# Performance work log

Hardware: AMD Instinct MI355X
Metric: run time of the kernel (lower is better)

## Reference

```python
import jax, jax.numpy as jnp
import numpy as np

B, NQ, NK, E, H, F, L = 8, 300, 4096, 256, 8, 2048, 6
D = E // H
SCALE = D ** -0.5


def _ln(x, g, b):
    m = x.mean(-1, keepdims=True)
    v = ((x - m) ** 2).mean(-1, keepdims=True)
    return (x - m) / jnp.sqrt(v + 1e-5) * g + b


def _split_heads(x):
    b, n, _ = x.shape
    return x.reshape(b, n, H, D).transpose(0, 2, 1, 3)  # (B,H,N,D)


def _merge_heads(x):
    b, h, n, d = x.shape
    return x.transpose(0, 2, 1, 3).reshape(b, n, h * d)


def setup_inputs() -> dict:
    key = jax.random.key(0)
    c = [0]
    def nk():
        c[0] += 1
        return jax.random.fold_in(key, c[0])
    def p(shape):
        return jax.random.normal(nk(), shape, jnp.float32) * 0.02
    return {
        "tgt": jax.random.normal(nk(), (B, NQ, E), jnp.float32),
        "memory": jax.random.normal(nk(), (B, NK, E), jnp.float32),
        "geometry_mask": jax.random.randint(nk(), (B, NQ, NK), 0, 2).astype(bool),
        "sa_wqkv": p((L, 3 * E, E)), "sa_bqkv": p((L, 3 * E)),
        "sa_wo": p((L, E, E)), "sa_bo": p((L, E)),
        "ca_wq": p((L, E, E)), "ca_bq": p((L, E)),
        "ca_wk": p((L, E, E)), "ca_bk": p((L, E)),
        "ca_wv": p((L, E, E)), "ca_bv": p((L, E)),
        "ca_wo": p((L, E, E)), "ca_bo": p((L, E)),
        "f_w1": p((L, F, E)), "f_b1": p((L, F)),
        "f_w2": p((L, E, F)), "f_b2": p((L, E)),
        "ln1g": jnp.ones((L, E)), "ln1b": jnp.zeros((L, E)),
        "ln2g": jnp.ones((L, E)), "ln2b": jnp.zeros((L, E)),
        "ln3g": jnp.ones((L, E)), "ln3b": jnp.zeros((L, E)),
        "lnfg": jnp.ones((E,)), "lnfb": jnp.zeros((E,)),
    }


def _forward(tgt, memory, geometry_mask, params):
    mask4 = geometry_mask[:, None, :, :]  # (B,1,NQ,NK), broadcast over heads

    def step(t, p):
        (wqkv, bqkv, wo, bo, wq, bq, wk, bk, wv, bv, wco, bco,
         w1, b1, w2, b2, g1, be1, g2, be2, g3, be3) = p
        # --- self-attention (torch nn.MultiheadAttention, eval mode) ---
        qkv = t @ wqkv.T + bqkv
        q, k, v = jnp.split(qkv, 3, axis=-1)
        q, k, v = _split_heads(q), _split_heads(k), _split_heads(v)
        a = jax.nn.softmax(jnp.einsum('bhqd,bhkd->bhqk', q, k) * SCALE, axis=-1)
        sa = _merge_heads(jnp.einsum('bhqk,bhkd->bhqd', a, v)) @ wo.T + bo
        t = _ln(t + sa, g1, be1)
        # --- geometry-constrained cross-attention ---
        q = _split_heads(t @ wq.T + bq)
        k = _split_heads(memory @ wk.T + bk)
        v = _split_heads(memory @ wv.T + bv)
        s = jnp.einsum('bhqd,bhkd->bhqk', q, k) * SCALE
        s = jnp.where(mask4, s, -jnp.inf)  # masked_fill(~mask, -inf)
        a = jax.nn.softmax(s, axis=-1)
        ca = _merge_heads(jnp.einsum('bhqk,bhkd->bhqd', a, v)) @ wco.T + bco
        t = _ln(t + ca, g2, be2)
        # --- FFN ---
        f = jax.nn.relu(t @ w1.T + b1) @ w2.T + b2
        t = _ln(t + f, g3, be3)
        return t, None

    out, _ = jax.lax.scan(step, tgt, params)
    return out


def reference(tgt, memory, geometry_mask, sa_wqkv, sa_bqkv, sa_wo, sa_bo,
              ca_wq, ca_bq, ca_wk, ca_bk, ca_wv, ca_bv, ca_wo, ca_bo,
              f_w1, f_b1, f_w2, f_b2, ln1g, ln1b, ln2g, ln2b, ln3g, ln3b,
              lnfg, lnfb):
    params = (sa_wqkv, sa_bqkv, sa_wo, sa_bo, ca_wq, ca_bq, ca_wk, ca_bk,
              ca_wv, ca_bv, ca_wo, ca_bo, f_w1, f_b1, f_w2, f_b2,
              ln1g, ln1b, ln2g, ln2b, ln3g, ln3b)
    out = _forward(tgt, memory, geometry_mask, params)
    return _ln(out, lnfg, lnfb)
```

## Files before the change

kernel.cpp:

```cpp
#include <hip/hip_runtime.h>
#include <hip/hip_bf16.h>

constexpr int cB = 8, cNQ = 300, cNK = 4096, cE = 256, cH = 8, cD = 32, cF = 2048, cL = 6;
constexpr int MT = cB * cNQ;
constexpr int MM = cB * cNK;
constexpr int cQT = 10;
constexpr int cKS = 4;
constexpr float kScale = 0.17677669529663687f;

typedef __attribute__((ext_vector_type(8))) short short8_t;
typedef __attribute__((ext_vector_type(4))) short short4_t;
typedef __attribute__((ext_vector_type(4))) float float4_t;

__device__ inline short f2bf(float x) {
  __hip_bfloat16 h = __float2bfloat16(x);
  return __builtin_bit_cast(short, h);
}

__global__ void init_t(const float* __restrict__ in, float* __restrict__ t,
                       __hip_bfloat16* __restrict__ tb, int n) {
  int i = blockIdx.x * 256 + threadIdx.x;
  if (i < n) { float v = in[i]; t[i] = v; tb[i] = __float2bfloat16(v); }
}
__global__ void cast_f32_bf16(const float* __restrict__ in, __hip_bfloat16* __restrict__ out, int n) {
  int i = blockIdx.x * 256 + threadIdx.x;
  if (i < n) out[i] = __float2bfloat16(in[i]);
}

__global__ void pack_mask_T(const int* __restrict__ m, unsigned* __restrict__ mT) {
  int key = blockIdx.x * 256 + threadIdx.x;
  int qt = blockIdx.y, b = blockIdx.z;
  unsigned w = 0;
  for (int j = 0; j < 32; ++j) {
    int q = qt * 32 + j;
    unsigned bit = (q < cNQ) ? (unsigned)(m[((size_t)b * cNQ + q) * cNK + key] != 0) : 0u;
    w |= bit << j;
  }
  mT[((size_t)b * cQT + qt) * cNK + key] = w;
}

template<typename TA, typename TW, int EPI, int OMODE, typename TOUT>
__global__ __launch_bounds__(256) void gemm_mfma(const TA* __restrict__ A,
                                                 const TW* __restrict__ W,
                                                 const float* __restrict__ bias,
                                                 TOUT* __restrict__ C,
                                                 int M, int N, int K) {
  constexpr int LDSS = 72;
  __shared__ short As[64][LDSS];
  __shared__ short Ws[64][LDSS];
  int tid = threadIdx.x;
  int bm = blockIdx.x * 64, bn = blockIdx.y * 64;
  int lane = tid & 63, wave = tid >> 6;
  int m16 = lane & 15, quad = lane >> 4;
  int wm = (wave >> 1) * 32, wn = (wave & 1) * 32;

  int srow = tid >> 2;
  int kc = (tid & 3) * 16;
  bool aok = (bm + srow) < M;

  float4_t acc[2][2];
#pragma unroll
  for (int i = 0; i < 2; ++i)
#pragma unroll
    for (int j = 0; j < 2; ++j) acc[i][j] = (float4_t){0.f, 0.f, 0.f, 0.f};

  for (int k0 = 0; k0 < K; k0 += 64) {
    if constexpr (__hip_internal::is_same<TA, float>::value) {
      const float* src = A + (size_t)(bm + srow) * K + k0 + kc;
      short8_t p0, p1;
#pragma unroll
      for (int u = 0; u < 8; ++u) p0[u] = aok ? f2bf(src[u]) : (short)0;
#pragma unroll
      for (int u = 0; u < 8; ++u) p1[u] = aok ? f2bf(src[8 + u]) : (short)0;
      *(short8_t*)&As[srow][kc] = p0;
      *(short8_t*)&As[srow][kc + 8] = p1;
    } else {
      const TA* src = A + (size_t)(bm + srow) * K + k0 + kc;
      short8_t z = 0;
      *(short8_t*)&As[srow][kc] = aok ? *(const short8_t*)src : z;
      *(short8_t*)&As[srow][kc + 8] = aok ? *(const short8_t*)(src + 8) : z;
    }
    if constexpr (__hip_internal::is_same<TW, float>::value) {
      const float* src = W + (size_t)(bn + srow) * K + k0 + kc;
      short8_t p0, p1;
#pragma unroll
      for (int u = 0; u < 8; ++u) p0[u] = f2bf(src[u]);
#pragma unroll
      for (int u = 0; u < 8; ++u) p1[u] = f2bf(src[8 + u]);
      *(short8_t*)&Ws[srow][kc] = p0;
      *(short8_t*)&Ws[srow][kc + 8] = p1;
    } else {
      const TW* src = W + (size_t)(bn + srow) * K + k0 + kc;
      *(short8_t*)&Ws[srow][kc] = *(const short8_t*)src;
      *(short8_t*)&Ws[srow][kc + 8] = *(const short8_t*)(src + 8);
    }
    __syncthreads();
#pragma unroll
    for (int kk = 0; kk < 2; ++kk) {
      short8_t aF[2], bF[2];
#pragma unroll
      for (int i = 0; i < 2; ++i)
        aF[i] = *(const short8_t*)&As[wm + i * 16 + m16][kk * 32 + quad * 8];
#pragma unroll
      for (int j = 0; j < 2; ++j)
        bF[j] = *(const short8_t*)&Ws[wn + j * 16 + m16][kk * 32 + quad * 8];
#pragma unroll
      for (int i = 0; i < 2; ++i)
#pragma unroll
        for (int j = 0; j < 2; ++j)
          acc[i][j] = __builtin_amdgcn_mfma_f32_16x16x32_bf16(aF[i], bF[j], acc[i][j], 0, 0, 0);
    }
    __syncthreads();
  }

  if constexpr (OMODE == 2) {
#pragma unroll
    for (int i = 0; i < 2; ++i)
#pragma unroll
      for (int r = 0; r < 4; ++r) {
        int ml = wm + i * 16 + quad * 4 + r;
#pragma unroll
        for (int j = 0; j < 2; ++j) {
          int nl = wn + j * 16 + m16;
          Ws[nl][ml] = f2bf(acc[i][j][r] + bias[bn + nl]);
        }
      }
    __syncthreads();
    int nl = tid >> 2, mc = (tid & 3) * 16;
    if (bm + mc < M) {
      int n = bn + nl;
      __hip_bfloat16* dst = (__hip_bfloat16*)C +
          ((size_t)(n >> 5) * 32 + (n & 31)) * (size_t)M + bm + mc;
      *(short8_t*)dst = *(const short8_t*)&Ws[nl][mc];
      *(short8_t*)(dst + 8) = *(const short8_t*)&Ws[nl][mc + 8];
    }
  } else {
#pragma unroll
    for (int i = 0; i < 2; ++i) {
#pragma unroll
      for (int r = 0; r < 4; ++r) {
        int m = bm + wm + i * 16 + quad * 4 + r;
        if (m >= M) continue;
#pragma unroll
        for (int j = 0; j < 2; ++j) {
          int n = bn + wn + j * 16 + m16;
          float v = acc[i][j][r] + bias[n];
          if (EPI == 1) v = fmaxf(v, 0.f);
          if constexpr (OMODE == 1) {
            ((__hip_bfloat16*)C)[((size_t)(n >> 5) * M + m) * 32 + (n & 31)] = __float2bfloat16(v);
          } else if constexpr (__hip_internal::is_same<TOUT, float>::value) {
            C[(size_t)m * N + n] = v;
          } else {
            C[(size_t)m * N + n] = __float2bfloat16(v);
          }
        }
      }
    }
  }
}

template<typename TW, int EPI, int OMODE, typename TOUT>
__global__ __launch_bounds__(256) void gemm128(const __hip_bfloat16* __restrict__ A,
                                               const TW* __restrict__ W,
                                               const float* __restrict__ bias,
                                               TOUT* __restrict__ C,
                                               int M, int N, int K) {
  __shared__ short lds[2 * 128 * 72];
  auto As = (short(*)[72])lds;
  auto Ws = (short(*)[72])(lds + 128 * 72);
  int tid = threadIdx.x;
  int bm = blockIdx.x * 128, bn = blockIdx.y * 128;
  int lane = tid & 63, wave = tid >> 6;
  int n16 = lane & 15, quad = lane >> 4;
  int wm = (wave >> 1) * 64, wn = (wave & 1) * 64;
  int srow = tid >> 1, kc = (tid & 1) * 32;
  bool aok = (bm + srow) < M;

  float4_t acc[4][4];
#pragma unroll
  for (int i = 0; i < 4; ++i)
#pragma unroll
    for (int j = 0; j < 4; ++j) acc[i][j] = (float4_t){0.f, 0.f, 0.f, 0.f};

  for (int k0 = 0; k0 < K; k0 += 64) {
    {
      const __hip_bfloat16* src = A + (size_t)(bm + srow) * K + k0 + kc;
      short8_t z = 0;
#pragma unroll
      for (int u = 0; u < 4; ++u)
        *(short8_t*)&As[srow][kc + u * 8] = aok ? *(const short8_t*)(src + u * 8) : z;
    }
    if constexpr (__hip_internal::is_same<TW, float>::value) {
      const float* src = W + (size_t)(bn + srow) * K + k0 + kc;
#pragma unroll
      for (int u = 0; u < 4; ++u) {
        short8_t p;
#pragma unroll
        for (int v = 0; v < 8; ++v) p[v] = f2bf(src[u * 8 + v]);
        *(short8_t*)&Ws[srow][kc + u * 8] = p;
      }
    } else {
      const TW* src = W + (size_t)(bn + srow) * K + k0 + kc;
#pragma unroll
      for (int u = 0; u < 4; ++u)
        *(short8_t*)&Ws[srow][kc + u * 8] = *(const short8_t*)(src + u * 8);
    }
    __syncthreads();
#pragma unroll
    for (int kk = 0; kk < 2; ++kk) {
      short8_t aF[4], bF[4];
#pragma unroll
      for (int i = 0; i < 4; ++i)
        aF[i] = *(const short8_t*)&As[wm + i * 16 + n16][kk * 32 + quad * 8];
#pragma unroll
      for (int j = 0; j < 4; ++j)
        bF[j] = *(const short8_t*)&Ws[wn + j * 16 + n16][kk * 32 + quad * 8];
#pragma unroll
      for (int i = 0; i < 4; ++i)
#pragma unroll
        for (int j = 0; j < 4; ++j)
          acc[i][j] = __builtin_amdgcn_mfma_f32_16x16x32_bf16(aF[i], bF[j], acc[i][j], 0, 0, 0);
    }
    __syncthreads();
  }

  if constexpr (OMODE == 2) {
    auto TT = (short(*)[128])lds;
#pragma unroll
    for (int i = 0; i < 4; ++i)
#pragma unroll
      for (int r = 0; r < 4; ++r) {
        int ml = wm + i * 16 + quad * 4 + r;
#pragma unroll
        for (int j = 0; j < 4; ++j) {
          int nl = wn + j * 16 + n16;
          TT[nl][ml] = f2bf(acc[i][j][r] + bias[bn + nl]);
        }
      }
    __syncthreads();
    int nl = tid >> 1, mh = (tid & 1) * 64;
    int n = bn + nl;
    __hip_bfloat16* dst = (__hip_bfloat16*)C +
        ((size_t)(n >> 5) * 32 + (n & 31)) * (size_t)M + bm + mh;
#pragma unroll
    for (int ch = 0; ch < 8; ++ch) {
      if (bm + mh + ch * 8 < M)
        *(short8_t*)(dst + ch * 8) = *(const short8_t*)&TT[nl][mh + ch * 8];
    }
  } else {
#pragma unroll
    for (int i = 0; i < 4; ++i) {
#pragma unroll
      for (int r = 0; r < 4; ++r) {
        int m = bm + wm + i * 16 + quad * 4 + r;
        if (m >= M) continue;
#pragma unroll
        for (int j = 0; j < 4; ++j) {
          int n = bn + wn + j * 16 + n16;
          float v = acc[i][j][r] + bias[n];
          if (EPI == 1) v = fmaxf(v, 0.f);
          if constexpr (OMODE == 1) {
            ((__hip_bfloat16*)C)[((size_t)(n >> 5) * M + m) * 32 + (n & 31)] = __float2bfloat16(v);
          } else if constexpr (__hip_internal::is_same<TOUT, float>::value) {
            C[(size_t)m * N + n] = v;
          } else {
            C[(size_t)m * N + n] = __float2bfloat16(v);
          }
        }
      }
    }
  }
}

template<typename TQ, bool MASKED>
__global__ __launch_bounds__(64, 4) void attn_flash(
    const TQ* __restrict__ qb, size_t strQb, size_t strQh, int qRowStr,
    const __hip_bfloat16* __restrict__ kb, size_t strKb, size_t strKh, int kRowStr,
    const __hip_bfloat16* __restrict__ vt, size_t strVb, size_t strVh, size_t strVd,
    const unsigned* __restrict__ mT, size_t strMb,
    float* __restrict__ pO, size_t pStrO,
    float* __restrict__ pL, size_t pStrL,
    int nq, int nk, int kChunk) {
  int hb = blockIdx.x;
  int h = hb & 7, bz = hb >> 3;
  int qt = blockIdx.y, ks = blockIdx.z;
  int qbase = qt * 32;

  const TQ* q = qb + (size_t)bz * strQb + (size_t)h * strQh;
  const __hip_bfloat16* K = kb + (size_t)bz * strKb + (size_t)h * strKh;
  const __hip_bfloat16* V = vt + (size_t)bz * strVb + (size_t)h * strVh;
  const unsigned* mrow = MASKED ? (mT + (size_t)bz * strMb + (size_t)qt * cNK) : nullptr;

  int lane = threadIdx.x;
  int n16 = lane & 15, quad = lane >> 4;

  __shared__ short sP[32][40];

  short8_t qf[2];
#pragma unroll
  for (int qi = 0; qi < 2; ++qi) {
    qf[qi] = 0;
    int qr = qbase + qi * 16 + n16;
    if (qr < nq) {
      const TQ* qp = q + (size_t)qr * qRowStr + quad * 8;
      if constexpr (__hip_internal::is_same<TQ, float>::value) {
#pragma unroll
        for (int j = 0; j < 8; ++j) qf[qi][j] = f2bf(qp[j]);
      } else {
        qf[qi] = *(const short8_t*)qp;
      }
    }
  }
  short8_t ones;
#pragma unroll
  for (int j = 0; j < 8; ++j) ones[j] = f2bf(1.0f);

  float4_t accO[2][2], accL[2];
#pragma unroll
  for (int qi = 0; qi < 2; ++qi) {
    accL[qi] = (float4_t){0.f, 0.f, 0.f, 0.f};
#pragma unroll
    for (int di = 0; di < 2; ++di) accO[qi][di] = (float4_t){0.f, 0.f, 0.f, 0.f};
  }
  float4_t zero4 = {0.f, 0.f, 0.f, 0.f};

  int kbeg = ks * kChunk;
  int kend = kbeg + kChunk;
  if (kend > ((nk + 31) & ~31)) kend = (nk + 31) & ~31;
  for (int koff = kbeg; koff < kend; koff += 32) {
    int k0 = koff + 2 * n16;
    unsigned w0 = 0xFFFFFFFFu, w1 = 0xFFFFFFFFu;
    if (MASKED) {
      const unsigned* mp = mrow + k0;
      w0 = mp[0]; w1 = mp[1];
    }
    bool in0 = k0 < nk, in1 = (k0 + 1) < nk;
    short8_t kf0 = *(const short8_t*)(K + (size_t)k0 * kRowStr + quad * 8);
    short8_t kf1 = *(const short8_t*)(K + (size_t)(k0 + 1) * kRowStr + quad * 8);
    short8_t vf0 = *(const short8_t*)(V + (size_t)n16 * strVd + koff + quad * 8);
    short8_t vf1 = *(const short8_t*)(V + (size_t)(16 + n16) * strVd + koff + quad * 8);
    float4_t s00 = __builtin_amdgcn_mfma_f32_16x16x32_bf16(qf[0], kf0, zero4, 0, 0, 0);
    float4_t s01 = __builtin_amdgcn_mfma_f32_16x16x32_bf16(qf[0], kf1, zero4, 0, 0, 0);
    float4_t s10 = __builtin_amdgcn_mfma_f32_16x16x32_bf16(qf[1], kf0, zero4, 0, 0, 0);
    float4_t s11 = __builtin_amdgcn_mfma_f32_16x16x32_bf16(qf[1], kf1, zero4, 0, 0, 0);
#pragma unroll
    for (int qi = 0; qi < 2; ++qi) {
      const float4_t& sa = qi ? s10 : s00;
      const float4_t& sb = qi ? s11 : s01;
#pragma unroll
      for (int r = 0; r < 4; ++r) {
        int row = qi * 16 + quad * 4 + r;
        bool ok0 = in0, ok1 = in1;
        if (MASKED) {
          ok0 = ok0 && ((w0 >> row) & 1u);
          ok1 = ok1 && ((w1 >> row) & 1u);
        }
        float p0 = ok0 ? __expf(sa[r] * kScale) : 0.f;
        float p1 = ok1 ? __expf(sb[r] * kScale) : 0.f;
        unsigned pw = (unsigned)(unsigned short)f2bf(p0) |
                      ((unsigned)(unsigned short)f2bf(p1) << 16);
        *(unsigned*)&sP[row][2 * n16] = pw;
      }
    }
#pragma unroll
    for (int qi = 0; qi < 2; ++qi) {
      short8_t pf = *(const short8_t*)&sP[qi * 16 + n16][quad * 8];
      accO[qi][0] = __builtin_amdgcn_mfma_f32_16x16x32_bf16(pf, vf0, accO[qi][0], 0, 0, 0);
      accO[qi][1] = __builtin_amdgcn_mfma_f32_16x16x32_bf16(pf, vf1, accO[qi][1], 0, 0, 0);
      accL[qi]    = __builtin_amdgcn_mfma_f32_16x16x32_bf16(pf, ones, accL[qi], 0, 0, 0);
    }
  }

  size_t oBase = (size_t)ks * pStrO + (size_t)(bz * cNQ) * 256 + h * 32;
  size_t lBase = (size_t)ks * pStrL + (size_t)hb * 320;
#pragma unroll
  for (int qi = 0; qi < 2; ++qi) {
#pragma unroll
    for (int r = 0; r < 4; ++r) {
      int row = qi * 16 + quad * 4 + r;
      if (qbase + row >= nq) continue;
#pragma unroll
      for (int di = 0; di < 2; ++di)
        pO[oBase + (size_t)(qbase + row) * 256 + di * 16 + n16] = accO[qi][di][r];
      if (n16 == 0) pL[lBase + qbase + row] = accL[qi][r];
    }
  }
}

__global__ __launch_bounds__(64) void attn_merge(const float* __restrict__ pO,
                                                 const float* __restrict__ pL,
                                                 __hip_bfloat16* __restrict__ out) {
  int row = blockIdx.x;
  int lane = threadIdx.x;
  int c0 = lane * 4;
  int bz = row / cNQ, qq = row - bz * cNQ;
  int h = c0 >> 5;
  float l = 0.f;
#pragma unroll
  for (int ks = 0; ks < cKS; ++ks)
    l += pL[(size_t)ks * (64 * 320) + (size_t)(bz * 8 + h) * 320 + qq];
  float inv = 1.f / l;
  float o[4] = {0.f, 0.f, 0.f, 0.f};
#pragma unroll
  for (int ks = 0; ks < cKS; ++ks) {
    const float4_t v = *(const float4_t*)&pO[(size_t)ks * (MT * 256) + (size_t)row * 256 + c0];
#pragma unroll
    for (int u = 0; u < 4; ++u) o[u] += v[u];
  }
  short4_t res = {f2bf(o[0] * inv), f2bf(o[1] * inv), f2bf(o[2] * inv), f2bf(o[3] * inv)};
  *(short4_t*)&out[(size_t)row * 256 + c0] = res;
}

__global__ __launch_bounds__(64) void add_ln_k(float* __restrict__ t,
                                               __hip_bfloat16* __restrict__ tb,
                                               const float* __restrict__ delta,
                                               const float* __restrict__ g,
                                               const float* __restrict__ bb) {
  int r = blockIdx.x, lane = threadIdx.x;
  size_t base = (size_t)r * cE + lane * 4;
  float x[4];
  float s = 0.f;
#pragma unroll
  for (int i = 0; i < 4; ++i) { x[i] = t[base + i] + delta[base + i]; s += x[i]; }
  for (int off = 32; off; off >>= 1) s += __shfl_xor(s, off);
  float mean = s * (1.f / cE);
  float v = 0.f;
#pragma unroll
  for (int i = 0; i < 4; ++i) { float dd = x[i] - mean; v += dd * dd; }
  for (int off = 32; off; off >>= 1) v += __shfl_xor(v, off);
  float rstd = rsqrtf(v * (1.f / cE) + 1e-5f);
  float y[4];
#pragma unroll
  for (int i = 0; i < 4; ++i) {
    y[i] = (x[i] - mean) * rstd * g[lane * 4 + i] + bb[lane * 4 + i];
    t[base + i] = y[i];
  }
  short4_t pb = {f2bf(y[0]), f2bf(y[1]), f2bf(y[2]), f2bf(y[3])};
  *(short4_t*)&tb[base] = pb;
}

__global__ __launch_bounds__(64) void final_ln_k(const float* __restrict__ t,
                                                 const float* __restrict__ g,
                                                 const float* __restrict__ bb,
                                                 float* __restrict__ out) {
  int r = blockIdx.x, lane = threadIdx.x;
  size_t base = (size_t)r * cE + lane * 4;
  float x[4];
  float s = 0.f;
#pragma unroll
  for (int i = 0; i < 4; ++i) { x[i] = t[base + i]; s += x[i]; }
  for (int off = 32; off; off >>= 1) s += __shfl_xor(s, off);
  float mean = s * (1.f / cE);
  float v = 0.f;
#pragma unroll
  for (int i = 0; i < 4; ++i) { float dd = x[i] - mean; v += dd * dd; }
  for (int off = 32; off; off >>= 1) v += __shfl_xor(v, off);
  float rstd = rsqrtf(v * (1.f / cE) + 1e-5f);
#pragma unroll
  for (int i = 0; i < 4; ++i)
    out[base + i] = (x[i] - mean) * rstd * g[lane * 4 + i] + bb[lane * 4 + i];
}

struct Bufs {
  float *t, *s1, *s2, *pO, *pL;
  __hip_bfloat16 *tb, *big2, *vtq, *s1b, *s2b, *qbf, *ffnh, *kbuf, *vtb, *membf;
  unsigned* mTr;
  const float* memory;
  bool fullKV, precast;
};

template<typename TW>
static void run_layers(const TW* const* wt, const float* const* bs,
                       const float* ln1g, const float* ln1b,
                       const float* ln2g, const float* ln2b,
                       const float* ln3g, const float* ln3b,
                       Bufs B, hipStream_t stream) {
  const size_t pStrO = (size_t)MT * 256, pStrL = 64 * 320;
  for (int l = 0; l < cL; ++l) {
    const TW* wqkv = wt[0] + (size_t)l * 3 * cE * cE;  const float* bqkv = bs[0] + (size_t)l * 3 * cE;
    const TW* wo   = wt[1] + (size_t)l * cE * cE;      const float* bo   = bs[1] + (size_t)l * cE;
    const TW* wq   = wt[2] + (size_t)l * cE * cE;      const float* bq   = bs[2] + (size_t)l * cE;
    const TW* wk   = wt[3] + (size_t)l * cE * cE;      const float* bk   = bs[3] + (size_t)l * cE;
    const TW* wv   = wt[4] + (size_t)l * cE * cE;      const float* bv   = bs[4] + (size_t)l * cE;
    const TW* wco  = wt[5] + (size_t)l * cE * cE;      const float* bco  = bs[5] + (size_t)l * cE;
    const TW* w1   = wt[6] + (size_t)l * cF * cE;      const float* b1   = bs[6] + (size_t)l * cF;
    const TW* w2   = wt[7] + (size_t)l * cE * cF;      const float* b2   = bs[7] + (size_t)l * cE;

    gemm_mfma<__hip_bfloat16, TW, 0, 0, __hip_bfloat16><<<dim3(38, 8), 256, 0, stream>>>(
        B.tb, wqkv, bqkv, B.big2, MT, 512, cE);
    gemm_mfma<__hip_bfloat16, TW, 0, 2, __hip_bfloat16><<<dim3(38, 4), 256, 0, stream>>>(
        B.tb, wqkv + (size_t)512 * cE, bqkv + 512, B.vtq, MT, cE, cE);
    attn_flash<__hip_bfloat16, false><<<dim3(64, cQT, cKS), 64, 0, stream>>>(
        B.big2, (size_t)cNQ * 512, 32, 512,
        B.big2 + 256, (size_t)cNQ * 512, 32, 512,
        B.vtq, 300, (size_t)cD * MT, MT,
        nullptr, 0,
        B.pO, pStrO, B.pL, pStrL, cNQ, cNQ, 96);
    attn_merge<<<MT, 64, 0, stream>>>(B.pO, B.pL, B.s1b);
    gemm_mfma<__hip_bfloat16, TW, 0, 0, float><<<dim3(38, 4), 256, 0, stream>>>(
        B.s1b, wo, bo, B.s2, MT, cE, cE);
    add_ln_k<<<MT, 64, 0, stream>>>(B.t, B.tb, B.s2, ln1g + (size_t)l * cE, ln1b + (size_t)l * cE);
    gemm_mfma<__hip_bfloat16, TW, 0, 0, __hip_bfloat16><<<dim3(38, 4), 256, 0, stream>>>(
        B.tb, wq, bq, B.qbf, MT, cE, cE);
    if (B.fullKV && B.precast) {
      gemm128<TW, 0, 1, __hip_bfloat16><<<dim3(256, 2), 256, 0, stream>>>(
          B.membf, wk, bk, B.kbuf, MM, cE, cE);
      gemm128<TW, 0, 2, __hip_bfloat16><<<dim3(256, 2), 256, 0, stream>>>(
          B.membf, wv, bv, B.vtb, MM, cE, cE);
      attn_flash<__hip_bfloat16, true><<<dim3(64, cQT, cKS), 64, 0, stream>>>(
          B.qbf, (size_t)cNQ * cE, 32, cE,
          B.kbuf, (size_t)cNK * cD, (size_t)MM * cD, cD,
          B.vtb, (size_t)cNK, (size_t)cD * MM, MM,
          B.mTr, (size_t)cQT * cNK,
          B.pO, pStrO, B.pL, pStrL, cNQ, cNK, 1024);
      attn_merge<<<MT, 64, 0, stream>>>(B.pO, B.pL, B.s2b);
    } else {
      for (int b = 0; b < cB; ++b) {
        const float* memb = B.memory + (size_t)b * cNK * cE;
        gemm_mfma<float, TW, 0, 1, __hip_bfloat16><<<dim3(64, 4), 256, 0, stream>>>(
            memb, wk, bk, B.kbuf, cNK, cE, cE);
        gemm_mfma<float, TW, 0, 2, __hip_bfloat16><<<dim3(64, 4), 256, 0, stream>>>(
            memb, wv, bv, B.vtb, cNK, cE, cE);
        attn_flash<__hip_bfloat16, true><<<dim3(8, cQT, cKS), 64, 0, stream>>>(
            B.qbf + (size_t)b * cNQ * cE, 0, 32, cE,
            B.kbuf, 0, (size_t)cNK * cD, cD,
            B.vtb, 0, (size_t)cD * cNK, cNK,
            B.mTr + (size_t)b * cQT * cNK, 0,
            B.pO + (size_t)b * cNQ * 256, pStrO, B.pL + (size_t)b * 8 * 320, pStrL,
            cNQ, cNK, 1024);
      }
      attn_merge<<<MT, 64, 0, stream>>>(B.pO, B.pL, B.s2b);
    }
    gemm_mfma<__hip_bfloat16, TW, 0, 0, float><<<dim3(38, 4), 256, 0, stream>>>(
        B.s2b, wco, bco, B.s1, MT, cE, cE);
    add_ln_k<<<MT, 64, 0, stream>>>(B.t, B.tb, B.s1, ln2g + (size_t)l * cE, ln2b + (size_t)l * cE);
    gemm128<TW, 1, 0, __hip_bfloat16><<<dim3(19, 16), 256, 0, stream>>>(
        B.tb, w1, b1, B.ffnh, MT, cF, cE);
    gemm_mfma<__hip_bfloat16, TW, 0, 0, float><<<dim3(38, 4), 256, 0, stream>>>(
        B.ffnh, w2, b2, B.s1, MT, cE, cF);
    add_ln_k<<<MT, 64, 0, stream>>>(B.t, B.tb, B.s1, ln3g + (size_t)l * cE, ln3b + (size_t)l * cE);
  }
}

extern "C" void kernel_launch(void* const* d_in, const int* in_sizes, int n_in,
                              void* d_out, int out_size, void* d_ws, size_t ws_size,
                              hipStream_t stream) {
  (void)in_sizes; (void)n_in; (void)out_size;
  const float* tgt    = (const float*)d_in[0];
  const float* memory = (const float*)d_in[1];
  const int*   gmask  = (const int*)d_in[2];
  const float* w_in[8]  = {(const float*)d_in[3], (const float*)d_in[5], (const float*)d_in[7],
                           (const float*)d_in[9], (const float*)d_in[11], (const float*)d_in[13],
                           (const float*)d_in[15], (const float*)d_in[17]};
  const float* b_in[8]  = {(const float*)d_in[4], (const float*)d_in[6], (const float*)d_in[8],
                           (const float*)d_in[10], (const float*)d_in[12], (const float*)d_in[14],
                           (const float*)d_in[16], (const float*)d_in[18]};
  const size_t w_sz[8]  = {(size_t)cL*3*cE*cE, (size_t)cL*cE*cE, (size_t)cL*cE*cE,
                           (size_t)cL*cE*cE, (size_t)cL*cE*cE, (size_t)cL*cE*cE,
                           (size_t)cL*cF*cE, (size_t)cL*cE*cF};
  const float* ln1g = (const float*)d_in[19], *ln1b = (const float*)d_in[20];
  const float* ln2g = (const float*)d_in[21], *ln2b = (const float*)d_in[22];
  const float* ln3g = (const float*)d_in[23], *ln3b = (const float*)d_in[24];
  const float* lnfg = (const float*)d_in[25], *lnfb = (const float*)d_in[26];

  char* wp = (char*)d_ws;
  auto alloc = [&](size_t bytes) { void* p = wp; wp += (bytes + 255) & ~(size_t)255; return p; };

  Bufs B;
  B.memory = memory;
  B.t  = (float*)alloc((size_t)MT * cE * 4);
  B.s1 = (float*)alloc((size_t)MT * cE * 4);
  B.s2 = (float*)alloc((size_t)MT * cE * 4);
  B.tb = (__hip_bfloat16*)alloc((size_t)MT * cE * 2);
  B.big2 = (__hip_bfloat16*)alloc((size_t)MT * 512 * 2);
  B.vtq  = (__hip_bfloat16*)alloc((size_t)cH * cD * MT * 2);
  B.mTr = (unsigned*)alloc((size_t)cB * cQT * cNK * 4);
  B.pO = (float*)alloc((size_t)cKS * MT * 256 * 4);
  B.pL = (float*)alloc((size_t)cKS * 64 * 320 * 4);
  B.s1b = B.big2;
  B.s2b = B.big2 + (size_t)MT * 256;
  B.qbf = (__hip_bfloat16*)B.s1;
  B.ffnh = (__hip_bfloat16*)B.pO;

  size_t kvFull = (size_t)cH * MM * cD * 2;
  size_t used = (size_t)(wp - (char*)d_ws);
  B.fullKV = ws_size >= used + 2 * kvFull;
  if (B.fullKV) {
    B.kbuf = (__hip_bfloat16*)alloc(kvFull);
    B.vtb  = (__hip_bfloat16*)alloc(kvFull);
  } else {
    B.kbuf = (__hip_bfloat16*)alloc((size_t)cH * cNK * cD * 2);
    B.vtb  = (__hip_bfloat16*)alloc((size_t)cH * cNK * cD * 2);
  }
  size_t memBytes = (size_t)MM * cE * 2;
  used = (size_t)(wp - (char*)d_ws);
  B.precast = B.fullKV && (ws_size >= used + memBytes);
  B.membf = B.precast ? (__hip_bfloat16*)alloc(memBytes) : nullptr;

  size_t wbfTotal = 0;
  for (int i = 0; i < 8; ++i) wbfTotal += ((w_sz[i] * 2 + 255) & ~(size_t)255);
  used = (size_t)(wp - (char*)d_ws);
  bool wPre = ws_size >= used + wbfTotal;
  __hip_bfloat16* wbf[8] = {};
  if (wPre)
    for (int i = 0; i < 8; ++i) wbf[i] = (__hip_bfloat16*)alloc(w_sz[i] * 2);

  init_t<<<(MT * cE + 255) / 256, 256, 0, stream>>>(tgt, B.t, B.tb, MT * cE);
  pack_mask_T<<<dim3(cNK / 256, cQT, cB), 256, 0, stream>>>(gmask, B.mTr);
  if (B.precast)
    cast_f32_bf16<<<(MM * cE + 255) / 256, 256, 0, stream>>>(memory, B.membf, MM * cE);
  if (wPre)
    for (int i = 0; i < 8; ++i)
      cast_f32_bf16<<<(int)((w_sz[i] + 255) / 256), 256, 0, stream>>>(w_in[i], wbf[i], (int)w_sz[i]);

  if (wPre) {
    const __hip_bfloat16* wt[8];
    for (int i = 0; i < 8; ++i) wt[i] = wbf[i];
    run_layers<__hip_bfloat16>(wt, b_in, ln1g, ln1b, ln2g, ln2b, ln3g, ln3b, B, stream);
  } else {
    run_layers<float>(w_in, b_in, ln1g, ln1b, ln2g, ln2b, ln3g, ln3b, B, stream);
  }

  final_ln_k<<<MT, 64, 0, stream>>>(B.t, lnfg, lnfb, (float*)d_out);
}
```

Measured before the change: 1.268 ms.

## Fuse split-K attention merge into output GEMM, merge K/V GEMMs, prefetch attention tiles

Removes the separate attn_merge kernel by having the output-projection GEMM sum partial O and L across key splits and normalize while loading its A tile. It also merges the K and V projection GEMMs into one launch, raises the cross-attention key-split count from 4 to 8 with smaller chunks, and software-prefetches the next K/V/mask fragments in the flash loop. The exponent becomes exp2 with a folded constant, and bf16 packing uses integer rounding. These aim to cut launch count, intermediate traffic and load latency, at the cost of larger partial buffers and redundant merge work repeated across the N-blocks of the GEMM.

New measurement: 1.409 ms. 11.1% more time.

```diff
diff --git a/kernel.cpp b/kernel.cpp
--- a/kernel.cpp
+++ b/kernel.cpp
@@ -5,8 +5,12 @@
 constexpr int MT = cB * cNQ;
 constexpr int MM = cB * cNK;
 constexpr int cQT = 10;
-constexpr int cKS = 4;
+constexpr int cKSc = 8;
+constexpr int cKSs = 4;
 constexpr float kScale = 0.17677669529663687f;
+constexpr float kE = 0.25509966355953075f;
+constexpr size_t pStrO = (size_t)MT * 256;
+constexpr size_t pStrL = 64 * 320;
 
 typedef __attribute__((ext_vector_type(8))) short short8_t;
 typedef __attribute__((ext_vector_type(4))) short short4_t;
@@ -39,12 +43,13 @@
   mT[((size_t)b * cQT + qt) * cNK + key] = w;
 }
 
-template<typename TA, typename TW, int EPI, int OMODE, typename TOUT>
+template<typename TA, typename TW, int EPI, int OMODE, typename TOUT, int NKS>
 __global__ __launch_bounds__(256) void gemm_mfma(const TA* __restrict__ A,
                                                  const TW* __restrict__ W,
                                                  const float* __restrict__ bias,
                                                  TOUT* __restrict__ C,
-                                                 int M, int N, int K) {
+                                                 int M, int N, int K,
+                                                 const float* __restrict__ pL) {
   constexpr int LDSS = 72;
   __shared__ short As[64][LDSS];
   __shared__ short Ws[64][LDSS];
@@ -65,7 +70,37 @@
     for (int j = 0; j < 2; ++j) acc[i][j] = (float4_t){0.f, 0.f, 0.f, 0.f};
 
   for (int k0 = 0; k0 < K; k0 += 64) {
-    if constexpr (__hip_internal::is_same<TA, float>::value) {
+    if constexpr (NKS > 0) {
+      const float* pO = (const float*)A;
+      short8_t p0 = 0, p1 = 0;
+      if (aok) {
+        int m = bm + srow;
+        int bz = m / cNQ, qq = m - bz * cNQ;
+        int h = (k0 + kc) >> 5;
+        float l = 0.f;
+#pragma unroll
+        for (int ks = 0; ks < NKS; ++ks)
+          l += pL[(size_t)ks * pStrL + (size_t)(bz * 8 + h) * 320 + qq];
+        float inv = 1.f / l;
+        float v[16];
+#pragma unroll
+        for (int c = 0; c < 4; ++c) {
+          float4_t sum = {0.f, 0.f, 0.f, 0.f};
+#pragma unroll
+          for (int ks = 0; ks < NKS; ++ks) {
+            float4_t x = *(const float4_t*)&pO[(size_t)ks * pStrO + (size_t)m * 256 + k0 + kc + c * 4];
+#pragma unroll
+            for (int u = 0; u < 4; ++u) sum[u] += x[u];
+          }
+#pragma unroll
+          for (int u = 0; u < 4; ++u) v[c * 4 + u] = sum[u] * inv;
+        }
+#pragma unroll
+        for (int u = 0; u < 8; ++u) { p0[u] = f2bf(v[u]); p1[u] = f2bf(v[8 + u]); }
+      }
+      *(short8_t*)&As[srow][kc] = p0;
+      *(short8_t*)&As[srow][kc + 8] = p1;
+    } else if constexpr (__hip_internal::is_same<TA, float>::value) {
       const float* src = A + (size_t)(bm + srow) * K + k0 + kc;
       short8_t p0, p1;
 #pragma unroll
@@ -159,7 +194,7 @@
   }
 }
 
-template<typename TW, int EPI, int OMODE, typename TOUT>
+template<typename TW, int EPI, typename TOUT>
 __global__ __launch_bounds__(256) void gemm128(const __hip_bfloat16* __restrict__ A,
                                                const TW* __restrict__ W,
                                                const float* __restrict__ bias,
@@ -224,7 +259,105 @@
     __syncthreads();
   }
 
-  if constexpr (OMODE == 2) {
+#pragma unroll
+  for (int i = 0; i < 4; ++i) {
+#pragma unroll
+    for (int r = 0; r < 4; ++r) {
+      int m = bm + wm + i * 16 + quad * 4 + r;
+      if (m >= M) continue;
+#pragma unroll
+      for (int j = 0; j < 4; ++j) {
+        int n = bn + wn + j * 16 + n16;
+        float v = acc[i][j][r] + bias[n];
+        if (EPI == 1) v = fmaxf(v, 0.f);
+        if constexpr (__hip_internal::is_same<TOUT, float>::value)
+          C[(size_t)m * N + n] = v;
+        else
+          C[(size_t)m * N + n] = __float2bfloat16(v);
+      }
+    }
+  }
+}
+
+template<typename TA, typename TW>
+__global__ __launch_bounds__(256) void gemm_kv(const TA* __restrict__ A,
+                                               const TW* __restrict__ Wk, const TW* __restrict__ Wv,
+                                               const float* __restrict__ bk, const float* __restrict__ bv,
+                                               __hip_bfloat16* __restrict__ Ck,
+                                               __hip_bfloat16* __restrict__ Cv,
+                                               int M, int K) {
+  __shared__ short lds[2 * 128 * 72];
+  auto As = (short(*)[72])lds;
+  auto Ws = (short(*)[72])(lds + 128 * 72);
+  bool isV = blockIdx.z == 1;
+  const TW* W = isV ? Wv : Wk;
+  const float* bias = isV ? bv : bk;
+  int tid = threadIdx.x;
+  int bm = blockIdx.x * 128, bn = blockIdx.y * 128;
+  int lane = tid & 63, wave = tid >> 6;
+  int n16 = lane & 15, quad = lane >> 4;
+  int wm = (wave >> 1) * 64, wn = (wave & 1) * 64;
+  int srow = tid >> 1, kc = (tid & 1) * 32;
+  bool aok = (bm + srow) < M;
+
+  float4_t acc[4][4];
+#pragma unroll
+  for (int i = 0; i < 4; ++i)
+#pragma unroll
+    for (int j = 0; j < 4; ++j) acc[i][j] = (float4_t){0.f, 0.f, 0.f, 0.f};
+
+  for (int k0 = 0; k0 < K; k0 += 64) {
+    if constexpr (__hip_internal::is_same<TA, float>::value) {
+      const float* src = A + (size_t)(bm + srow) * K + k0 + kc;
+#pragma unroll
+      for (int u = 0; u < 4; ++u) {
+        short8_t p;
+#pragma unroll
+        for (int v = 0; v < 8; ++v) p[v] = aok ? f2bf(src[u * 8 + v]) : (short)0;
+        *(short8_t*)&As[srow][kc + u * 8] = p;
+      }
+    } else {
+      const TA* src = A + (size_t)(bm + srow) * K + k0 + kc;
+      short8_t z = 0;
+#pragma unroll
+      for (int u = 0; u < 4; ++u)
+        *(short8_t*)&As[srow][kc + u * 8] = aok ? *(const short8_t*)(src + u * 8) : z;
+    }
+    if constexpr (__hip_internal::is_same<TW, float>::value) {
+      const float* src = W + (size_t)(bn + srow) * K + k0 + kc;
+#pragma unroll
+      for (int u = 0; u < 4; ++u) {
+        short8_t p;
+#pragma unroll
+        for (int v = 0; v < 8; ++v) p[v] = f2bf(src[u * 8 + v]);
+        *(short8_t*)&Ws[srow][kc + u * 8] = p;
+      }
+    } else {
+      const TW* src = W + (size_t)(bn + srow) * K + k0 + kc;
+#pragma unroll
+      for (int u = 0; u < 4; ++u)
+        *(short8_t*)&Ws[srow][kc + u * 8] = *(const short8_t*)(src + u * 8);
+    }
+    __syncthreads();
+#pragma unroll
+    for (int kk = 0; kk < 2; ++kk) {
+      short8_t aF[4], bF[4];
+#pragma unroll
+      for (int i = 0; i < 4; ++i)
+        aF[i] = *(const short8_t*)&As[wm + i * 16 + n16][kk * 32 + quad * 8];
+#pragma unroll
+      for (int j = 0; j < 4; ++j)
+        bF[j] = *(const short8_t*)&Ws[wn + j * 16 + n16][kk * 32 + quad * 8];
+#pragma unroll
+      for (int i = 0; i < 4; ++i)
+#pragma unroll
+        for (int j = 0; j < 4; ++j)
+          acc[i][j] = __builtin_amdgcn_mfma_f32_16x16x32_bf16(aF[i], bF[j], acc[i][j], 0, 0, 0);
+    }
+    __syncthreads();
+  }
+
+  if (isV) {
     auto TT = (short(*)[128])lds;
 #pragma unroll
     for (int i = 0; i < 4; ++i)
@@ -240,8 +373,7 @@
     __syncthreads();
     int nl = tid >> 1, mh = (tid & 1) * 64;
     int n = bn + nl;
-    __hip_bfloat16* dst = (__hip_bfloat16*)C +
-        ((size_t)(n >> 5) * 32 + (n & 31)) * (size_t)M + bm + mh;
+    __hip_bfloat16* dst = Cv + ((size_t)(n >> 5) * 32 + (n & 31)) * (size_t)M + bm + mh;
 #pragma unroll
     for (int ch = 0; ch < 8; ++ch) {
       if (bm + mh + ch * 8 < M)
@@ -258,14 +390,7 @@
         for (int j = 0; j < 4; ++j) {
           int n = bn + wn + j * 16 + n16;
           float v = acc[i][j][r] + bias[n];
-          if (EPI == 1) v = fmaxf(v, 0.f);
-          if constexpr (OMODE == 1) {
-            ((__hip_bfloat16*)C)[((size_t)(n >> 5) * M + m) * 32 + (n & 31)] = __float2bfloat16(v);
-          } else if constexpr (__hip_internal::is_same<TOUT, float>::value) {
-            C[(size_t)m * N + n] = v;
-          } else {
-            C[(size_t)m * N + n] = __float2bfloat16(v);
-          }
+          Ck[((size_t)(n >> 5) * M + m) * 32 + (n & 31)] = __float2bfloat16(v);
         }
       }
     }
@@ -278,8 +403,7 @@
     const __hip_bfloat16* __restrict__ kb, size_t strKb, size_t strKh, int kRowStr,
     const __hip_bfloat16* __restrict__ vt, size_t strVb, size_t strVh, size_t strVd,
     const unsigned* __restrict__ mT, size_t strMb,
-    float* __restrict__ pO, size_t pStrO,
-    float* __restrict__ pL, size_t pStrL,
+    float* __restrict__ pO, float* __restrict__ pL,
     int nq, int nk, int kChunk) {
   int hb = blockIdx.x;
   int h = hb & 7, bz = hb >> 3;
@@ -324,25 +448,43 @@
   }
   float4_t zero4 = {0.f, 0.f, 0.f, 0.f};
 
+  const __hip_bfloat16* Vb0 = V + (size_t)n16 * strVd;
+  const __hip_bfloat16* Vb1 = V + (size_t)(16 + n16) * strVd;
+
   int kbeg = ks * kChunk;
   int kend = kbeg + kChunk;
-  if (kend > ((nk + 31) & ~31)) kend = (nk + 31) & ~31;
+  int nkAl = (nk + 31) & ~31;
+  if (kend > nkAl) kend = nkAl;
+
+  short8_t kfA = 0, kfB = 0, vfA = 0, vfB = 0;
+  unsigned mwA = ~0u, mwB = ~0u;
+  if (kbeg < kend) {
+    int k0i = kbeg + 2 * n16;
+    kfA = *(const short8_t*)(K + (size_t)k0i * kRowStr + quad * 8);
+    kfB = *(const short8_t*)(K + (size_t)(k0i + 1) * kRowStr + quad * 8);
+    vfA = *(const short8_t*)(Vb0 + kbeg + quad * 8);
+    vfB = *(const short8_t*)(Vb1 + kbeg + quad * 8);
+    if (MASKED) { mwA = mrow[k0i]; mwB = mrow[k0i + 1]; }
+  }
+
   for (int koff = kbeg; koff < kend; koff += 32) {
-    int k0 = koff + 2 * n16;
-    unsigned w0 = 0xFFFFFFFFu, w1 = 0xFFFFFFFFu;
-    if (MASKED) {
-      const unsigned* mp = mrow + k0;
-      w0 = mp[0]; w1 = mp[1];
-    }
-    bool in0 = k0 < nk, in1 = (k0 + 1) < nk;
-    short8_t kf0 = *(const short8_t*)(K + (size_t)k0 * kRowStr + quad * 8);
-    short8_t kf1 = *(const short8_t*)(K + (size_t)(k0 + 1) * kRowStr + quad * 8);
-    short8_t vf0 = *(const short8_t*)(V + (size_t)n16 * strVd + koff + quad * 8);
-    short8_t vf1 = *(const short8_t*)(V + (size_t)(16 + n16) * strVd + koff + quad * 8);
-    float4_t s00 = __builtin_amdgcn_mfma_f32_16x16x32_bf16(qf[0], kf0, zero4, 0, 0, 0);
-    float4_t s01 = __builtin_amdgcn_mfma_f32_16x16x32_bf16(qf[0], kf1, zero4, 0, 0, 0);
-    float4_t s10 = __builtin_amdgcn_mfma_f32_16x16x32_bf16(qf[1], kf0, zero4, 0, 0, 0);
-    float4_t s11 = __builtin_amdgcn_mfma_f32_16x16x32_bf16(qf[1], kf1, zero4, 0, 0, 0);
+    short8_t kfA2 = 0, kfB2 = 0, vfA2 = 0, vfB2 = 0;
+    unsigned mwA2 = ~0u, mwB2 = ~0u;
+    int kn = koff + 32;
+    if (kn < kend) {
+      int k1i = kn + 2 * n16;
+      kfA2 = *(const short8_t*)(K + (size_t)k1i * kRowStr + quad * 8);
+      kfB2 = *(const short8_t*)(K + (size_t)(k1i + 1) * kRowStr + quad * 8);
+      vfA2 = *(const short8_t*)(Vb0 + kn + quad * 8);
+      vfB2 = *(const short8_t*)(Vb1 + kn + quad * 8);
+      if (MASKED) { mwA2 = mrow[k1i]; mwB2 = mrow[k1i + 1]; }
+    }
+    int k0i = koff + 2 * n16;
+    bool in0 = k0i < nk, in1 = (k0i + 1) < nk;
+    float4_t s00 = __builtin_amdgcn_mfma_f32_16x16x32_bf16(qf[0], kfA, zero4, 0, 0, 0);
+    float4_t s01 = __builtin_amdgcn_mfma_f32_16x16x32_bf16(qf[0], kfB, zero4, 0, 0, 0);
+    float4_t s10 = __builtin_amdgcn_mfma_f32_16x16x32_bf16(qf[1], kfA, zero4, 0, 0, 0);
+    float4_t s11 = __builtin_amdgcn_mfma_f32_16x16x32_bf16(qf[1], kfB, zero4, 0, 0, 0);
 #pragma unroll
     for (int qi = 0; qi < 2; ++qi) {
       const float4_t& sa = qi ? s10 : s00;
@@ -352,23 +494,25 @@
         int row = qi * 16 + quad * 4 + r;
         bool ok0 = in0, ok1 = in1;
         if (MASKED) {
-          ok0 = ok0 && ((w0 >> row) & 1u);
-          ok1 = ok1 && ((w1 >> row) & 1u);
+          ok0 = ok0 && ((mwA >> row) & 1u);
+          ok1 = ok1 && ((mwB >> row) & 1u);
         }
-        float p0 = ok0 ? __expf(sa[r] * kScale) : 0.f;
-        float p1 = ok1 ? __expf(sb[r] * kScale) : 0.f;
-        unsigned pw = (unsigned)(unsigned short)f2bf(p0) |
-                      ((unsigned)(unsigned short)f2bf(p1) << 16);
+        float p0 = ok0 ? exp2f(sa[r] * kE) : 0.f;
+        float p1 = ok1 ? exp2f(sb[r] * kE) : 0.f;
+        unsigned u0 = __builtin_bit_cast(unsigned, p0);
+        unsigned u1 = __builtin_bit_cast(unsigned, p1);
+        unsigned pw = ((u0 + 0x8000u) >> 16) | ((u1 + 0x8000u) & 0xFFFF0000u);
         *(unsigned*)&sP[row][2 * n16] = pw;
       }
     }
 #pragma unroll
     for (int qi = 0; qi < 2; ++qi) {
       short8_t pf = *(const short8_t*)&sP[qi * 16 + n16][quad * 8];
-      accO[qi][0] = __builtin_amdgcn_mfma_f32_16x16x32_bf16(pf, vf0, accO[qi][0], 0, 0, 0);
-      accO[qi][1] = __builtin_amdgcn_mfma_f32_16x16x32_bf16(pf, vf1, accO[qi][1], 0, 0, 0);
+      accO[qi][0] = __builtin_amdgcn_mfma_f32_16x16x32_bf16(pf, vfA, accO[qi][0], 0, 0, 0);
+      accO[qi][1] = __builtin_amdgcn_mfma_f32_16x16x32_bf16(pf, vfB, accO[qi][1], 0, 0, 0);
       accL[qi]    = __builtin_amdgcn_mfma_f32_16x16x32_bf16(pf, ones, accL[qi], 0, 0, 0);
     }
+    kfA = kfA2; kfB = kfB2; vfA = vfA2; vfB = vfB2; mwA = mwA2; mwB = mwB2;
   }
 
   size_t oBase = (size_t)ks * pStrO + (size_t)(bz * cNQ) * 256 + h * 32;
@@ -385,30 +529,6 @@
       if (n16 == 0) pL[lBase + qbase + row] = accL[qi][r];
     }
   }
-}
-
-__global__ __launch_bounds__(64) void attn_merge(const float* __restrict__ pO,
-                                                 const float* __restrict__ pL,
-                                                 __hip_bfloat16* __restrict__ out) {
-  int row = blockIdx.x;
-  int lane = threadIdx.x;
-  int c0 = lane * 4;
-  int bz = row / cNQ, qq = row - bz * cNQ;
-  int h = c0 >> 5;
-  float l = 0.f;
-#pragma unroll
-  for (int ks = 0; ks < cKS; ++ks)
-    l += pL[(size_t)ks * (64 * 320) + (size_t)(bz * 8 + h) * 320 + qq];
-  float inv = 1.f / l;
-  float o[4] = {0.f, 0.f, 0.f, 0.f};
-#pragma unroll
-  for (int ks = 0; ks < cKS; ++ks) {
-    const float4_t v = *(const float4_t*)&pO[(size_t)ks * (MT * 256) + (size_t)row * 256 + c0];
-#pragma unroll
-    for (int u = 0; u < 4; ++u) o[u] += v[u];
-  }
-  short4_t res = {f2bf(o[0] * inv), f2bf(o[1] * inv), f2bf(o[2] * inv), f2bf(o[3] * inv)};
-  *(short4_t*)&out[(size_t)row * 256 + c0] = res;
 }
 
 __global__ __launch_bounds__(64) void add_ln_k(float* __restrict__ t,
@@ -463,7 +583,7 @@
 
 struct Bufs {
   float *t, *s1, *s2, *pO, *pL;
-  __hip_bfloat16 *tb, *big2, *vtq, *s1b, *s2b, *qbf, *ffnh, *kbuf, *vtb, *membf;
+  __hip_bfloat16 *tb, *big2, *vtq, *qbf, *ffnh, *kbuf, *vtb, *membf;
   unsigned* mTr;
   const float* memory;
   bool fullKV, precast;
@@ -475,7 +595,6 @@
                        const float* ln2g, const float* ln2b,
                        const float* ln3g, const float* ln3b,
                        Bufs B, hipStream_t stream) {
-  const size_t pStrO = (size_t)MT * 256, pStrL = 64 * 320;
   for (int l = 0; l < cL; ++l) {
     const TW* wqkv = wt[0] + (size_t)l * 3 * cE * cE;  const float* bqkv = bs[0] + (size_t)l * 3 * cE;
     const TW* wo   = wt[1] + (size_t)l * cE * cE;      const float* bo   = bs[1] + (size_t)l * cE;
@@ -486,58 +605,57 @@
     const TW* w1   = wt[6] + (size_t)l * cF * cE;      const float* b1   = bs[6] + (size_t)l * cF;
     const TW* w2   = wt[7] + (size_t)l * cE * cF;      const float* b2   = bs[7] + (size_t)l * cE;
 
-    gemm_mfma<__hip_bfloat16, TW, 0, 0, __hip_bfloat16><<<dim3(38, 8), 256, 0, stream>>>(
-        B.tb, wqkv, bqkv, B.big2, MT, 512, cE);
-    gemm_mfma<__hip_bfloat16, TW, 0, 2, __hip_bfloat16><<<dim3(38, 4), 256, 0, stream>>>(
-        B.tb, wqkv + (size_t)512 * cE, bqkv + 512, B.vtq, MT, cE, cE);
-    attn_flash<__hip_bfloat16, false><<<dim3(64, cQT, cKS), 64, 0, stream>>>(
+    gemm_mfma<__hip_bfloat16, TW, 0, 0, __hip_bfloat16, 0><<<dim3(38, 8), 256, 0, stream>>>(
+        B.tb, wqkv, bqkv, B.big2, MT, 512, cE, nullptr);
+    gemm_mfma<__hip_bfloat16, TW, 0, 2, __hip_bfloat16, 0><<<dim3(38, 4), 256, 0, stream>>>(
+        B.tb, wqkv + (size_t)512 * cE, bqkv + 512, B.vtq, MT, cE, cE, nullptr);
+    attn_flash<__hip_bfloat16, false><<<dim3(64, cQT, cKSs), 64, 0, stream>>>(
         B.big2, (size_t)cNQ * 512, 32, 512,
         B.big2 + 256, (size_t)cNQ * 512, 32, 512,
         B.vtq, 300, (size_t)cD * MT, MT,
         nullptr, 0,
-        B.pO, pStrO, B.pL, pStrL, cNQ, cNQ, 96);
-    attn_merge<<<MT, 64, 0, stream>>>(B.pO, B.pL, B.s1b);
-    gemm_mfma<__hip_bfloat16, TW, 0, 0, float><<<dim3(38, 4), 256, 0, stream>>>(
-        B.s1b, wo, bo, B.s2, MT, cE, cE);
+        B.pO, B.pL, cNQ, cNQ, 96);
+    gemm_mfma<float, TW, 0, 0, float, cKSs><<<dim3(38, 4), 256, 0, stream>>>(
+        B.pO, wo, bo, B.s2, MT, cE, cE, B.pL);
     add_ln_k<<<MT, 64, 0, stream>>>(B.t, B.tb, B.s2, ln1g + (size_t)l * cE, ln1b + (size_t)l * cE);
-    gemm_mfma<__hip_bfloat16, TW, 0, 0, __hip_bfloat16><<<dim3(38, 4), 256, 0, stream>>>(
-        B.tb, wq, bq, B.qbf, MT, cE, cE);
-    if (B.fullKV && B.precast) {
-      gemm128<TW, 0, 1, __hip_bfloat16><<<dim3(256, 2), 256, 0, stream>>>(
-          B.membf, wk, bk, B.kbuf, MM, cE, cE);
-      gemm128<TW, 0, 2, __hip_bfloat16><<<dim3(256, 2), 256, 0, stream>>>(
-          B.membf, wv, bv, B.vtb, MM, cE, cE);
-      attn_flash<__hip_bfloat16, true><<<dim3(64, cQT, cKS), 64, 0, stream>>>(
+    gemm_mfma<__hip_bfloat16, TW, 0, 0, __hip_bfloat16, 0><<<dim3(38, 4), 256, 0, stream>>>(
+        B.tb, wq, bq, B.qbf, MT, cE, cE, nullptr);
+    if (B.fullKV) {
+      if (B.precast)
+        gemm_kv<__hip_bfloat16, TW><<<dim3(256, 2, 2), 256, 0, stream>>>(
+            B.membf, wk, wv, bk, bv, B.kbuf, B.vtb, MM, cE);
+      else
+        gemm_kv<float, TW><<<dim3(256, 2, 2), 256, 0, stream>>>(
+            B.memory, wk, wv, bk, bv, B.kbuf, B.vtb, MM, cE);
+      attn_flash<__hip_bfloat16, true><<<dim3(64, cQT, cKSc), 64, 0, stream>>>(
           B.qbf, (size_t)cNQ * cE, 32, cE,
           B.kbuf, (size_t)cNK * cD, (size_t)MM * cD, cD,
           B.vtb, (size_t)cNK, (size_t)cD * MM, MM,
           B.mTr, (size_t)cQT * cNK,
-          B.pO, pStrO, B.pL, pStrL, cNQ, cNK, 1024);
-      attn_merge<<<MT, 64, 0, stream>>>(B.pO, B.pL, B.s2b);
+          B.pO, B.pL, cNQ, cNK, 512);
     } else {
       for (int b = 0; b < cB; ++b) {
         const float* memb = B.memory + (size_t)b * cNK * cE;
-        gemm_mfma<float, TW, 0, 1, __hip_bfloat16><<<dim3(64, 4), 256, 0, stream>>>(
-            memb, wk, bk, B.kbuf, cNK, cE, cE);
-        gemm_mfma<float, TW, 0, 2, __hip_bfloat16><<<dim3(64, 4), 256, 0, stream>>>(
-            memb, wv, bv, B.vtb, cNK, cE, cE);
-        attn_flash<__hip_bfloat16, true><<<dim3(8, cQT, cKS), 64, 0, stream>>>(
+        gemm_mfma<float, TW, 0, 1, __hip_bfloat16, 0><<<dim3(64, 4), 256, 0, stream>>>(
+            memb, wk, bk, B.kbuf, cNK, cE, cE, nullptr);
+        gemm_mfma<float, TW, 0, 2, __hip_bfloat16, 0><<<dim3(64, 4), 256, 0, stream>>>(
+            memb, wv, bv, B.vtb, cNK, cE, cE, nullptr);
+        attn_flash<__hip_bfloat16, true><<<dim3(8, cQT, cKSc), 64, 0, stream>>>(
             B.qbf + (size_t)b * cNQ * cE, 0, 32, cE,
             B.kbuf, 0, (size_t)cNK * cD, cD,
             B.vtb, 0, (size_t)cD * cNK, cNK,
             B.mTr + (size_t)b * cQT * cNK, 0,
-            B.pO + (size_t)b * cNQ * 256, pStrO, B.pL + (size_t)b * 8 * 320, pStrL,
-            cNQ, cNK, 1024);
-      }
-      attn_merge<<<MT, 64, 0, stream>>>(B.pO, B.pL, B.s2b);
-    }
-    gemm_mfma<__hip_bfloat16, TW, 0, 0, float><<<dim3(38, 4), 256, 0, stream>>>(
-        B.s2b, wco, bco, B.s1, MT, cE, cE);
+            B.pO + (size_t)b * cNQ * 256, B.pL + (size_t)b * 8 * 320,
+            cNQ, cNK, 512);
+      }
+    }
+    gemm_mfma<float, TW, 0, 0, float, cKSc><<<dim3(38, 4), 256, 0, stream>>>(
+        B.pO, wco, bco, B.s1, MT, cE, cE, B.pL);
     add_ln_k<<<MT, 64, 0, stream>>>(B.t, B.tb, B.s1, ln2g + (size_t)l * cE, ln2b + (size_t)l * cE);
-    gemm128<TW, 1, 0, __hip_bfloat16><<<dim3(19, 16), 256, 0, stream>>>(
+    gemm128<TW, 1, __hip_bfloat16><<<dim3(19, 16), 256, 0, stream>>>(
         B.tb, w1, b1, B.ffnh, MT, cF, cE);
-    gemm_mfma<__hip_bfloat16, TW, 0, 0, float><<<dim3(38, 4), 256, 0, stream>>>(
-        B.ffnh, w2, b2, B.s1, MT, cE, cF);
+    gemm_mfma<__hip_bfloat16, TW, 0, 0, float, 0><<<dim3(38, 4), 256, 0, stream>>>(
+        B.ffnh, w2, b2, B.s1, MT, cE, cF, nullptr);
     add_ln_k<<<MT, 64, 0, stream>>>(B.t, B.tb, B.s1, ln3g + (size_t)l * cE, ln3b + (size_t)l * cE);
   }
 }
@@ -575,10 +693,8 @@
   B.big2 = (__hip_bfloat16*)alloc((size_t)MT * 512 * 2);
   B.vtq  = (__hip_bfloat16*)alloc((size_t)cH * cD * MT * 2);
   B.mTr = (unsigned*)alloc((size_t)cB * cQT * cNK * 4);
-  B.pO = (float*)alloc((size_t)cKS * MT * 256 * 4);
-  B.pL = (float*)alloc((size_t)cKS * 64 * 320 * 4);
-  B.s1b = B.big2;
-  B.s2b = B.big2 + (size_t)MT * 256;
+  B.pO = (float*)alloc((size_t)cKSc * MT * 256 * 4);
+  B.pL = (float*)alloc((size_t)cKSc * 64 * 320 * 4);
   B.qbf = (__hip_bfloat16*)B.s1;
   B.ffnh = (__hip_bfloat16*)B.pO;
 
```
